# Performance work log

Hardware: AMD Instinct MI355X
Metric: run time of the kernel (lower is better)

## Reference

```python
import jax, jax.numpy as jnp
import numpy as np

PI = 3.14159265358979323846
MARGIN = 6.0
DIM = 256
ENT_TOT = 43234
REL_RANGE = (6.0 + 2.0) / DIM  # (margin + epsilon) / dim = 0.03125


def setup_inputs() -> dict:
    key = jax.random.key(0)
    k1, k2, k3 = jax.random.split(key, 3)
    head = jax.random.normal(k1, (32, 2 * DIM), dtype=jnp.float32)
    relation = jax.random.normal(k2, (32, DIM), dtype=jnp.float32)
    ent_emb = jax.random.normal(k3, (ENT_TOT, 2 * DIM), dtype=jnp.float32)
    return {"head": head, "relation": relation, "ent_emb": ent_emb}


def reference(head, relation, ent_emb):
    # head: (B, 2D) -> re/im halves (B, D)
    re_h, im_h = jnp.split(head, 2, axis=-1)
    # entity table: (E, 2D) -> (E, D) each
    re_t, im_t = jnp.split(ent_emb, 2, axis=-1)
    # phase rotation from relation embedding
    phase = relation / (REL_RANGE / PI)          # (B, D)
    re_r = jnp.cos(phase)
    im_r = jnp.sin(phase)
    # complex rotation of head by relation: (B, D)
    re_rot = re_h * re_r - im_h * im_r
    im_rot = re_h * im_r + im_h * re_r
    # difference against every entity, broadcast to (B, E, D)
    re_s = re_rot[:, None, :] - re_t[None, :, :]
    im_s = im_rot[:, None, :] - im_t[None, :, :]
    # L2 norm over the complex pair, summed over D -> (B, E)
    dist = jnp.sqrt(re_s * re_s + im_s * im_s).sum(axis=-1)
    return MARGIN - dist
```

## Files before the change

kernel.cpp:

```cpp
#include <hip/hip_runtime.h>
#include <math.h>

#define DIMH 256
#define NB   32
#define E_TOT 43234
#define TE   32
#define DK   32
#define NC   (DIMH / DK)
#define PHASE_DIV 0.009947183943243459f

typedef float v2f __attribute__((ext_vector_type(2)));
typedef float v4f __attribute__((ext_vector_type(4)));

__global__ __launch_bounds__(256) void rot_kernel(const float* __restrict__ head,
                                                  const float* __restrict__ rel,
                                                  float4* __restrict__ rot_v4) {
    int i  = blockIdx.x * 256 + threadIdx.x;
    int b  = i >> 7;
    int dp = i & 127;
    int d0 = dp * 2;
    float4 w;
    {
        float re_h = head[b * 2 * DIMH + d0];
        float im_h = head[b * 2 * DIMH + DIMH + d0];
        float s, c;
        sincosf(rel[b * DIMH + d0] / PHASE_DIV, &s, &c);
        w.x = re_h * c - im_h * s;
        w.z = re_h * s + im_h * c;
    }
    {
        float re_h = head[b * 2 * DIMH + d0 + 1];
        float im_h = head[b * 2 * DIMH + DIMH + d0 + 1];
        float s, c;
        sincosf(rel[b * DIMH + d0 + 1] / PHASE_DIV, &s, &c);
        w.y = re_h * c - im_h * s;
        w.w = re_h * s + im_h * c;
    }
    rot_v4[b * (DIMH / 2) + dp] = w;
}

__device__ __forceinline__ v2f sqrt2(v2f s) {
    v2f r;
    r.x = __builtin_amdgcn_sqrtf(s.x);
    r.y = __builtin_amdgcn_sqrtf(s.y);
    return r;
}

__global__ __launch_bounds__(256, 6) void dist_kernel(const float* __restrict__ ent,
                                                      const float4* __restrict__ rot_v4,
                                                      float* __restrict__ out) {
    __shared__ v4f s_e[TE][DK / 2 + 1];
    __shared__ v4f s_r[NB][DK / 2 + 1];

    const int tid = threadIdx.x;
    const int eb  = blockIdx.x * TE;
    const int ep  = tid & 15;
    const int bp  = tid >> 4;

    const int srow = tid >> 3;
    const int c4   = tid & 7;
    const int er   = min(eb + srow, E_TOT - 1);
    const int rrow = tid >> 4;
    const int rdp  = tid & 15;

    float4 p_re, p_im, p_r0, p_r1;

    auto load_chunk = [&](int c) {
        const int dk = c * DK;
        const float* b0 = &ent[(size_t)er * (2 * DIMH)];
        p_re = *reinterpret_cast<const float4*>(b0 + dk + 4 * c4);
        p_im = *reinterpret_cast<const float4*>(b0 + DIMH + dk + 4 * c4);
        p_r0 = rot_v4[rrow * (DIMH / 2) + c * (DK / 2) + rdp];
        p_r1 = rot_v4[(rrow + 16) * (DIMH / 2) + c * (DK / 2) + rdp];
    };

    v2f acc[2][2];
    #pragma unroll
    for (int j = 0; j < 2; ++j)
        #pragma unroll
        for (int k = 0; k < 2; ++k) { acc[j][k].x = 0.f; acc[j][k].y = 0.f; }

    load_chunk(0);

    for (int c = 0; c < NC; ++c) {
        {
            v4f lo, hi;
            lo.x = p_re.x; lo.y = p_re.y; lo.z = p_im.x; lo.w = p_im.y;
            hi.x = p_re.z; hi.y = p_re.w; hi.z = p_im.z; hi.w = p_im.w;
            s_e[srow][2 * c4]     = lo;
            s_e[srow][2 * c4 + 1] = hi;
            v4f r0, r1;
            r0.x = p_r0.x; r0.y = p_r0.y; r0.z = p_r0.z; r0.w = p_r0.w;
            r1.x = p_r1.x; r1.y = p_r1.y; r1.z = p_r1.z; r1.w = p_r1.w;
            s_r[rrow][rdp]      = r0;
            s_r[rrow + 16][rdp] = r1;
        }
        __syncthreads();

        if (c + 1 < NC) load_chunk(c + 1);

        #pragma unroll 4
        for (int p = 0; p < DK / 2; ++p) {
            v4f r0 = s_r[2 * bp][p];
            v4f r1 = s_r[2 * bp + 1][p];
            v4f e0 = s_e[ep][p];
            v4f e1 = s_e[ep + 16][p];

            {   v2f a = r0.xy - e0.xy, b = r0.zw - e0.zw;
                acc[0][0] += sqrt2(a * a + b * b); }
            {   v2f a = r0.xy - e1.xy, b = r0.zw - e1.zw;
                acc[0][1] += sqrt2(a * a + b * b); }
            {   v2f a = r1.xy - e0.xy, b = r1.zw - e0.zw;
                acc[1][0] += sqrt2(a * a + b * b); }
            {   v2f a = r1.xy - e1.xy, b = r1.zw - e1.zw;
                acc[1][1] += sqrt2(a * a + b * b); }
        }
        __syncthreads();
    }

    #pragma unroll
    for (int k = 0; k < 2; ++k) {
        int e = eb + ep + 16 * k;
        if (e < E_TOT) {
            #pragma unroll
            for (int j = 0; j < 2; ++j)
                out[(size_t)(2 * bp + j) * E_TOT + e] = 6.0f - (acc[j][k].x + acc[j][k].y);
        }
    }
}

extern "C" void kernel_launch(void* const* d_in, const int* in_sizes, int n_in,
                              void* d_out, int out_size, void* d_ws, size_t ws_size,
                              hipStream_t stream) {
    const float* head = (const float*)d_in[0];
    const float* rel  = (const float*)d_in[1];
    const float* ent  = (const float*)d_in[2];
    float4* rot_v4 = (float4*)d_ws;

    rot_kernel<<<(NB * DIMH / 2) / 256, 256, 0, stream>>>(head, rel, rot_v4);

    int etiles = (E_TOT + TE - 1) / TE;
    dist_kernel<<<etiles, 256, 0, stream>>>(ent, rot_v4, (float*)d_out);
}
```

Measured before the change: 174.8 us.

## Keep rotated head in registers and reduce across dims with DPP

The distance kernel now stages only entity rows through shared memory. Each thread holds a fixed slice of the rotated head vectors for 4 batch rows in registers, and the per-entity sum over the dimension is done with a 32-lane DPP reduction instead of per-thread accumulation over all dims. This removes the repeated shared-memory traffic for rotated vectors and the double LDS reads per pair. The cost is more registers (occupancy hint lowered to 4), cross-lane reduction work per entity chunk, many single-lane scattered output writes, and smaller entity tiles per block.

```diff
diff --git a/kernel.cpp b/kernel.cpp
--- a/kernel.cpp
+++ b/kernel.cpp
@@ -4,13 +4,11 @@
 #define DIMH 256
 #define NB   32
 #define E_TOT 43234
-#define TE   32
-#define DK   32
-#define NC   (DIMH / DK)
+#define TE_B 16
+#define TE_C 2
 #define PHASE_DIV 0.009947183943243459f
 
 typedef float v2f __attribute__((ext_vector_type(2)));
-typedef float v4f __attribute__((ext_vector_type(4)));
 
 __global__ __launch_bounds__(256) void rot_kernel(const float* __restrict__ head,
                                                   const float* __restrict__ rel,
@@ -46,86 +44,99 @@
     return r;
 }
 
-__global__ __launch_bounds__(256, 6) void dist_kernel(const float* __restrict__ ent,
+__device__ __forceinline__ float dpp_reduce32(float h) {
+    h += __int_as_float(__builtin_amdgcn_update_dpp(0, __float_as_int(h), 0x111, 0xf, 0xf, true));
+    h += __int_as_float(__builtin_amdgcn_update_dpp(0, __float_as_int(h), 0x112, 0xf, 0xf, true));
+    h += __int_as_float(__builtin_amdgcn_update_dpp(0, __float_as_int(h), 0x114, 0xf, 0xf, true));
+    h += __int_as_float(__builtin_amdgcn_update_dpp(0, __float_as_int(h), 0x118, 0xf, 0xf, true));
+    h += __int_as_float(__builtin_amdgcn_update_dpp(0, __float_as_int(h), 0x142, 0xf, 0xf, true));
+    return h;
+}
+
+__global__ __launch_bounds__(256, 4) void dist_kernel(const float* __restrict__ ent,
                                                       const float4* __restrict__ rot_v4,
                                                       float* __restrict__ out) {
-    __shared__ v4f s_e[TE][DK / 2 + 1];
-    __shared__ v4f s_r[NB][DK / 2 + 1];
+    __shared__ float2 s_e[TE_C][8][32];
 
     const int tid = threadIdx.x;
-    const int eb  = blockIdx.x * TE;
-    const int ep  = tid & 15;
-    const int bp  = tid >> 4;
+    const int ds  = tid & 31;
+    const int bg  = tid >> 5;
+    const int eb  = blockIdx.x * TE_B;
 
-    const int srow = tid >> 3;
-    const int c4   = tid & 7;
-    const int er   = min(eb + srow, E_TOT - 1);
-    const int rrow = tid >> 4;
-    const int rdp  = tid & 15;
+    v2f rr[4][4], ri[4][4];
+    #pragma unroll
+    for (int jj = 0; jj < 4; ++jj) {
+        const int b = bg * 4 + jj;
+        #pragma unroll
+        for (int p = 0; p < 4; ++p) {
+            float4 w = rot_v4[b * (DIMH / 2) + ds * 4 + p];
+            rr[jj][p].x = w.x; rr[jj][p].y = w.y;
+            ri[jj][p].x = w.z; ri[jj][p].y = w.w;
+        }
+    }
 
-    float4 p_re, p_im, p_r0, p_r1;
+    const int e_l   = tid >> 7;
+    const int plane = (tid >> 6) & 1;
+    const int qd    = tid & 63;
 
-    auto load_chunk = [&](int c) {
-        const int dk = c * DK;
-        const float* b0 = &ent[(size_t)er * (2 * DIMH)];
-        p_re = *reinterpret_cast<const float4*>(b0 + dk + 4 * c4);
-        p_im = *reinterpret_cast<const float4*>(b0 + DIMH + dk + 4 * c4);
-        p_r0 = rot_v4[rrow * (DIMH / 2) + c * (DK / 2) + rdp];
-        p_r1 = rot_v4[(rrow + 16) * (DIMH / 2) + c * (DK / 2) + rdp];
+    float4 pf;
+    auto load_chunk = [&](int ch) {
+        int eg = min(eb + ch * TE_C + e_l, E_TOT - 1);
+        pf = *reinterpret_cast<const float4*>(&ent[(size_t)eg * (2 * DIMH) + plane * DIMH + 4 * qd]);
     };
-
-    v2f acc[2][2];
-    #pragma unroll
-    for (int j = 0; j < 2; ++j)
-        #pragma unroll
-        for (int k = 0; k < 2; ++k) { acc[j][k].x = 0.f; acc[j][k].y = 0.f; }
 
     load_chunk(0);
 
-    for (int c = 0; c < NC; ++c) {
+    for (int ch = 0; ch < TE_B / TE_C; ++ch) {
         {
-            v4f lo, hi;
-            lo.x = p_re.x; lo.y = p_re.y; lo.z = p_im.x; lo.w = p_im.y;
-            hi.x = p_re.z; hi.y = p_re.w; hi.z = p_im.z; hi.w = p_im.w;
-            s_e[srow][2 * c4]     = lo;
-            s_e[srow][2 * c4 + 1] = hi;
-            v4f r0, r1;
-            r0.x = p_r0.x; r0.y = p_r0.y; r0.z = p_r0.z; r0.w = p_r0.w;
-            r1.x = p_r1.x; r1.y = p_r1.y; r1.z = p_r1.z; r1.w = p_r1.w;
-            s_r[rrow][rdp]      = r0;
-            s_r[rrow + 16][rdp] = r1;
+            const int dsw = qd >> 1;
+            const int u0  = ((qd & 1) ? 2 : 0) + plane * 4;
+            float2 lo, hi;
+            lo.x = pf.x; lo.y = pf.y;
+            hi.x = pf.z; hi.y = pf.w;
+            s_e[e_l][u0][dsw]     = lo;
+            s_e[e_l][u0 + 1][dsw] = hi;
         }
         __syncthreads();
 
-        if (c + 1 < NC) load_chunk(c + 1);
+        if (ch + 1 < TE_B / TE_C) load_chunk(ch + 1);
 
-        #pragma unroll 4
-        for (int p = 0; p < DK / 2; ++p) {
-            v4f r0 = s_r[2 * bp][p];
-            v4f r1 = s_r[2 * bp + 1][p];
-            v4f e0 = s_e[ep][p];
-            v4f e1 = s_e[ep + 16][p];
+        v2f acc[4][TE_C];
+        #pragma unroll
+        for (int jj = 0; jj < 4; ++jj)
+            #pragma unroll
+            for (int ee = 0; ee < TE_C; ++ee) { acc[jj][ee].x = 0.f; acc[jj][ee].y = 0.f; }
 
-            {   v2f a = r0.xy - e0.xy, b = r0.zw - e0.zw;
-                acc[0][0] += sqrt2(a * a + b * b); }
-            {   v2f a = r0.xy - e1.xy, b = r0.zw - e1.zw;
-                acc[0][1] += sqrt2(a * a + b * b); }
-            {   v2f a = r1.xy - e0.xy, b = r1.zw - e0.zw;
-                acc[1][0] += sqrt2(a * a + b * b); }
-            {   v2f a = r1.xy - e1.xy, b = r1.zw - e1.zw;
-                acc[1][1] += sqrt2(a * a + b * b); }
+        #pragma unroll
+        for (int ee = 0; ee < TE_C; ++ee) {
+            v2f er[4], ei[4];
+            #pragma unroll
+            for (int p = 0; p < 4; ++p) {
+                float2 a = s_e[ee][p][ds];
+                float2 b = s_e[ee][p + 4][ds];
+                er[p].x = a.x; er[p].y = a.y;
+                ei[p].x = b.x; ei[p].y = b.y;
+            }
+            #pragma unroll
+            for (int jj = 0; jj < 4; ++jj)
+                #pragma unroll
+                for (int p = 0; p < 4; ++p) {
+                    v2f a = rr[jj][p] - er[p];
+                    v2f b = ri[jj][p] - ei[p];
+                    acc[jj][ee] += sqrt2(a * a + b * b);
+                }
         }
         __syncthreads();
-    }
 
-    #pragma unroll
-    for (int k = 0; k < 2; ++k) {
-        int e = eb + ep + 16 * k;
-        if (e < E_TOT) {
+        #pragma unroll
+        for (int jj = 0; jj < 4; ++jj)
             #pragma unroll
-            for (int j = 0; j < 2; ++j)
-                out[(size_t)(2 * bp + j) * E_TOT + e] = 6.0f - (acc[j][k].x + acc[j][k].y);
-        }
+            for (int ee = 0; ee < TE_C; ++ee) {
+                float h = dpp_reduce32(acc[jj][ee].x + acc[jj][ee].y);
+                const int e = eb + ch * TE_C + ee;
+                if ((tid & 31) == 31 && e < E_TOT)
+                    out[(size_t)(bg * 4 + jj) * E_TOT + e] = 6.0f - h;
+            }
     }
 }
 
@@ -139,6 +150,6 @@
 
     rot_kernel<<<(NB * DIMH / 2) / 256, 256, 0, stream>>>(head, rel, rot_v4);
 
-    int etiles = (E_TOT + TE - 1) / TE;
-    dist_kernel<<<etiles, 256, 0, stream>>>(ent, rot_v4, (float*)d_out);
+    int eblocks = (E_TOT + TE_B - 1) / TE_B;
+    dist_kernel<<<eblocks, 256, 0, stream>>>(ent, rot_v4, (float*)d_out);
 }
```

Result: no change. 176.3 us (+0.8%).
